# Kernel optimization log

Measured on AMD Instinct MI355X. Metric: run time of the kernel, lower is better.

Reference implementation:

```python
import jax, jax.numpy as jnp
import numpy as np

D = 128          # embedding_dim
L = 3            # gnn layers
P = 100          # num_predicate_classes
C = 50           # num_object_classes
AR = 3           # arity
A = 16           # num_actions
NVB = 200_000    # boolean variables
NVN = 100_000    # numeric variables
NF = 100_000     # factors (objects)
EB = 400_000     # boolean edges
EN = 200_000     # numeric edges


def setup_inputs() -> dict:
    key = jax.random.key(0)
    ks = jax.random.split(key, 24)
    s = 1.0 / np.sqrt(D)
    inp = {
        # boolean subgraph
        "var_type_bool": jax.random.randint(ks[0], (NVB,), 0, P),
        "var_value_bool": jax.random.randint(ks[1], (NVB,), 0, 2),
        # numeric subgraph
        "var_type_num": jax.random.randint(ks[2], (NVN,), 0, P),
        "var_value_num": jax.random.normal(ks[3], (NVN,), dtype=jnp.float32),
        # factors
        "factor_class": jax.random.randint(ks[4], (NF,), 0, C),
        # edges (sender = variable idx, receiver = factor idx, attr = arity slot)
        "senders_bool": jax.random.randint(ks[5], (EB,), 0, NVB),
        "receivers_bool": jax.random.randint(ks[6], (EB,), 0, NF),
        "edge_type_bool": jax.random.randint(ks[7], (EB,), 0, AR),
        "senders_num": jax.random.randint(ks[8], (EN,), 0, NVN),
        "receivers_num": jax.random.randint(ks[9], (EN,), 0, NF),
        "edge_type_num": jax.random.randint(ks[10], (EN,), 0, AR),
        "action_mask": jax.random.randint(ks[11], (NF, A), 0, 2).astype(jnp.bool_),
        # learned parameters
        "pred_emb": jax.random.normal(ks[12], (P, D), dtype=jnp.float32) * s,
        "bool_emb": jax.random.normal(ks[13], (2, D), dtype=jnp.float32) * s,
        "fac_emb": jax.random.normal(ks[14], (C, D), dtype=jnp.float32) * s,
        "edge_emb": jax.random.normal(ks[15], (AR, D), dtype=jnp.float32) * s,
        "num_w": jax.random.normal(ks[16], (D,), dtype=jnp.float32) * s,
        "num_b": jnp.zeros((D,), dtype=jnp.float32),
        "W_msg_vf": jax.random.normal(ks[17], (L, D, D), dtype=jnp.float32) * s,
        "W_upd_f": jax.random.normal(ks[18], (L, 2 * D, D), dtype=jnp.float32) * s,
        "W_msg_fv": jax.random.normal(ks[19], (L, D, D), dtype=jnp.float32) * s,
        "W_upd_v": jax.random.normal(ks[20], (L, 2 * D, D), dtype=jnp.float32) * s,
        "W_pol": jax.random.normal(ks[21], (D, A), dtype=jnp.float32) * s,
        "b_pol": jnp.zeros((A,), dtype=jnp.float32),
    }
    return inp


def reference(var_type_bool, var_value_bool, var_type_num, var_value_num,
              factor_class, senders_bool, receivers_bool, edge_type_bool,
              senders_num, receivers_num, edge_type_num, action_mask,
              pred_emb, bool_emb, fac_emb, edge_emb, num_w, num_b,
              W_msg_vf, W_upd_f, W_msg_fv, W_upd_v, W_pol, b_pol):
    act = jax.nn.relu
    # ---- embed boolean variables: predicate embedding + boolean-value embedding
    v_bool = pred_emb[var_type_bool] + bool_emb[var_value_bool]        # [NVB, D]
    # ---- embed numeric variables: MLP on scalar value + predicate embedding
    v_num = act(var_value_num[:, None] * num_w + num_b) + pred_emb[var_type_num]  # [NVN, D]
    # ---- embed factors and edge attributes
    factors = fac_emb[factor_class]                                    # [NF, D]
    # ---- merge graphs: concat variables, offset numeric senders by n boolean vars
    n_vb = v_bool.shape[0]
    variables = jnp.concatenate([v_bool, v_num], axis=0)               # [NV, D]
    senders = jnp.concatenate([senders_bool, senders_num + n_vb])      # [E]
    receivers = jnp.concatenate([receivers_bool, receivers_num])       # [E]
    edge_attr = edge_emb[jnp.concatenate([edge_type_bool, edge_type_num])]  # [E, D]
    n_var = variables.shape[0]
    n_fac = factors.shape[0]
    # ---- bipartite GNN message passing (variable <-> factor)
    for l in range(L):
        # variable -> factor
        m_vf = act((variables[senders] + edge_attr) @ W_msg_vf[l])      # [E, D]
        agg_f = jax.ops.segment_sum(m_vf, receivers, num_segments=n_fac)
        factors = act(jnp.concatenate([factors, agg_f], axis=-1) @ W_upd_f[l])
        # factor -> variable
        m_fv = act((factors[receivers] + edge_attr) @ W_msg_fv[l])     # [E, D]
        agg_v = jax.ops.segment_sum(m_fv, senders, num_segments=n_var)
        variables = act(jnp.concatenate([variables, agg_v], axis=-1) @ W_upd_v[l])
    # ---- policy head: per-factor action logits, masked
    logits = factors @ W_pol + b_pol                                   # [NF, A]
    NEG = jnp.asarray(-1e9, dtype=logits.dtype)
    return jnp.where(action_mask, logits, NEG)
```

## Files before the change

kernel.cpp:

```cpp
#include <hip/hip_runtime.h>
#include <stdint.h>

#define D 128
#define NACT 16
#define LAYERS 3
#define SCH 8192

typedef __attribute__((ext_vector_type(4))) float f32x4;
typedef __attribute__((ext_vector_type(8))) short short8;

__device__ __forceinline__ unsigned short f2bf(float f) {
  union { float f; unsigned int u; } v; v.f = f;
  return (unsigned short)((v.u + 0x7fffu + ((v.u >> 16) & 1u)) >> 16);
}
__device__ __forceinline__ float bf2f(unsigned short s) {
  union { unsigned int u; float f; } v; v.u = ((unsigned int)s) << 16; return v.f;
}
__device__ __forceinline__ f32x4 mfma16(short8 a, short8 b, f32x4 c) {
  return __builtin_amdgcn_mfma_f32_16x16x32_bf16(a, b, c, 0, 0, 0);
}
__device__ __forceinline__ int SWZ(int row, int byteoff) {
  return (row * 256 + byteoff) ^ ((row & 7) << 4);
}

__device__ __forceinline__ void wave_barrier_lds() {
  asm volatile("s_waitcnt lgkmcnt(0)" ::: "memory");
  __builtin_amdgcn_s_barrier();
  __builtin_amdgcn_sched_barrier(0);
}

__device__ __forceinline__ void accum_edge(unsigned w, unsigned t,
                                           float e00, float e01, float e10, float e11,
                                           float e20, float e21, float& a0, float& a1) {
  float ee0 = (t == 0) ? e00 : ((t == 1) ? e10 : e20);
  float ee1 = (t == 0) ? e01 : ((t == 1) ? e11 : e21);
  float v0 = bf2f((unsigned short)(w & 0xFFFF)) + ee0;
  float v1 = bf2f((unsigned short)(w >> 16)) + ee1;
  a0 += v0 > 0.f ? v0 : 0.f;
  a1 += v1 > 0.f ? v1 : 0.f;
}

__global__ void k_setup(const float* __restrict__ Wvf, const float* __restrict__ Wfv,
                        const float* __restrict__ Wuf, const float* __restrict__ Wuv,
                        const float* __restrict__ Wpol, const float* __restrict__ femb,
                        const float* __restrict__ eemb,
                        const unsigned int* __restrict__ mask, int nMaskWords, int nFemb,
                        unsigned short* __restrict__ WvfT, unsigned short* __restrict__ WfvT,
                        unsigned short* __restrict__ WufT, unsigned short* __restrict__ WuvT,
                        unsigned short* __restrict__ WpT, unsigned short* __restrict__ fembB,
                        float* __restrict__ eWt, int* __restrict__ flag) {
  int tid = blockIdx.x * blockDim.x + threadIdx.x;
  int nthr = gridDim.x * blockDim.x;
  auto packT = [&](const float* src, unsigned short* dst, int Lc, int K, int N) {
    int total = Lc * K * N;
    for (int i = tid; i < total; i += nthr) {
      int l = i / (K * N);
      int rem = i - l * (K * N);
      int n = rem / K;
      int k = rem - n * K;
      dst[i] = f2bf(src[(l * K + k) * N + n]);
    }
  };
  packT(Wvf, WvfT, LAYERS, D, D);
  packT(Wfv, WfvT, LAYERS, D, D);
  packT(Wuf, WufT, LAYERS, 2 * D, D);
  packT(Wuv, WuvT, LAYERS, 2 * D, D);
  packT(Wpol, WpT, 1, D, NACT);
  for (int i = tid; i < nFemb; i += nthr) fembB[i] = f2bf(femb[i]);
  for (int o = tid; o < LAYERS * 2 * 3 * D; o += nthr) {
    int c = o & 127;
    int r = o >> 7;
    int t = r % 3; r /= 3;
    int dir = r & 1;
    int l = r >> 1;
    const float* W = (dir == 0 ? Wvf : Wfv) + (size_t)l * D * D;
    float s = 0.f;
    for (int k = 0; k < D; ++k) s += eemb[t * D + k] * W[k * D + c];
    eWt[o] = s;
  }
  int f = 0;
  for (int i = tid; i < nMaskWords; i += nthr) {
    unsigned w = mask[i];
    if (w > 1u) f |= 1;
    if (w > 0x01010101u) f |= 2;
  }
  if (f) atomicOr(flag, f);
}

__global__ void k_hist2(const int* __restrict__ rb, const int* __restrict__ rn,
                        const int* __restrict__ sb, const int* __restrict__ sn,
                        int EB, int EN, int NVB,
                        int* __restrict__ offR, int* __restrict__ offS) {
  int E = EB + EN;
  for (int e = blockIdx.x * blockDim.x + threadIdx.x; e < E; e += gridDim.x * blockDim.x) {
    int dR = (e < EB) ? rb[e] : rn[e - EB];
    atomicAdd(&offR[dR], 1);
    int dS = (e < EB) ? sb[e] : sn[e - EB] + NVB;
    atomicAdd(&offS[dS], 1);
  }
}

__global__ void k_scan_sums2(const int* __restrict__ offR, int nR, int* __restrict__ bsumR,
                             const int* __restrict__ offS, int nS, int* __restrict__ bsumS,
                             int nbR) {
  __shared__ int ts[256];
  const int* data; int n; int* bsum; int blk;
  if ((int)blockIdx.x < nbR) { data = offR; n = nR; bsum = bsumR; blk = blockIdx.x; }
  else { data = offS; n = nS; bsum = bsumS; blk = blockIdx.x - nbR; }
  int base = blk * SCH;
  int s = 0;
  for (int j = threadIdx.x; j < SCH; j += 256) {
    int i = base + j;
    if (i < n) s += data[i];
  }
  ts[threadIdx.x] = s;
  __syncthreads();
  if (threadIdx.x == 0) {
    int tot = 0;
    for (int i = 0; i < 256; ++i) tot += ts[i];
    bsum[blk] = tot;
  }
}

__global__ void k_scan_top2(int* __restrict__ bsumR, int nbR, int* __restrict__ offRend,
                            int* __restrict__ bsumS, int nbS, int* __restrict__ offSend,
                            int E) {
  if (threadIdx.x == 0) {
    int* bsum = (blockIdx.x == 0) ? bsumR : bsumS;
    int nb = (blockIdx.x == 0) ? nbR : nbS;
    int run = 0;
    for (int i = 0; i < nb; ++i) { int t = bsum[i]; bsum[i] = run; run += t; }
    if (blockIdx.x == 0) *offRend = E; else *offSend = E;
  }
}

__global__ void k_scan_apply2(int* __restrict__ offR, int nR, const int* __restrict__ bsumR,
                              int* __restrict__ offS, int nS, const int* __restrict__ bsumS,
                              int nbR) {
  __shared__ int ts[256];
  int* data; int n; const int* bsum; int blk;
  if ((int)blockIdx.x < nbR) { data = offR; n = nR; bsum = bsumR; blk = blockIdx.x; }
  else { data = offS; n = nS; bsum = bsumS; blk = blockIdx.x - nbR; }
  int base = blk * SCH + threadIdx.x * 32;
  int v[32];
  int s = 0;
#pragma unroll
  for (int j = 0; j < 32; ++j) {
    int i = base + j;
    v[j] = (i < n) ? data[i] : 0;
    s += v[j];
  }
  ts[threadIdx.x] = s;
  __syncthreads();
  if (threadIdx.x == 0) {
    int run = 0;
    for (int i = 0; i < 256; ++i) { int t = ts[i]; ts[i] = run; run += t; }
  }
  __syncthreads();
  int run = bsum[blk] + ts[threadIdx.x];
#pragma unroll
  for (int j = 0; j < 32; ++j) {
    run += v[j];
    int i = base + j;
    if (i < n) data[i] = run;
  }
}

__global__ void k_scatter2(const int* __restrict__ rb, const int* __restrict__ rn,
                           const int* __restrict__ sb, const int* __restrict__ sn,
                           const int* __restrict__ tb, const int* __restrict__ tn,
                           int EB, int EN, int NVB,
                           int* __restrict__ offR, unsigned* __restrict__ pkR,
                           int* __restrict__ offS, unsigned* __restrict__ pkS) {
  int E = EB + EN;
  for (int j = blockIdx.x * blockDim.x + threadIdx.x; j < 2 * E; j += gridDim.x * blockDim.x) {
    int d, s, t; int* off; unsigned* pk;
    if (j < E) {
      off = offR; pk = pkR;
      if (j < EB) { d = rb[j]; s = sb[j]; t = tb[j]; }
      else { int k = j - EB; d = rn[k]; s = sn[k] + NVB; t = tn[k]; }
    } else {
      int k2 = j - E;
      off = offS; pk = pkS;
      if (k2 < EB) { d = sb[k2]; s = rb[k2]; t = tb[k2]; }
      else { int k = k2 - EB; d = sn[k] + NVB; s = rn[k]; t = tn[k]; }
    }
    int pos = atomicAdd(&off[d], -1) - 1;
    pk[pos] = (unsigned)s | ((unsigned)t << 20);
  }
}

__global__ void __launch_bounds__(256)
k_emb_xw(const int* __restrict__ vtb, const int* __restrict__ vvb,
         const int* __restrict__ vtn, const float* __restrict__ vvn,
         const float* __restrict__ pred, const float* __restrict__ bemb,
         const float* __restrict__ numw, const float* __restrict__ numb,
         const unsigned short* __restrict__ WxT,
         unsigned short* __restrict__ vars, unsigned short* __restrict__ xw,
         int nvb, int nv) {
  __shared__ unsigned short LDSO[64 * 128];
  int wid = threadIdx.x >> 6, lane = threadIdx.x & 63;
  int r16 = lane & 15, g = lane >> 4;
  int rbase = blockIdx.x * 64 + wid * 16;
  char* ldso = (char*)LDSO + wid * 16 * 256;
  int c2 = lane * 2;

  float be00 = bemb[c2],     be01 = bemb[c2 + 1];
  float be10 = bemb[D + c2], be11 = bemb[D + c2 + 1];
  float nw0 = numw[c2], nw1 = numw[c2 + 1];
  float nb0 = numb[c2], nb1 = numb[c2 + 1];

  short8 bcur[4], bnxt[4];
#pragma unroll
  for (int ks = 0; ks < 4; ++ks)
    bcur[ks] = *(const short8*)(WxT + r16 * D + ks * 32 + g * 8);

#pragma unroll
  for (int h = 0; h < 2; ++h) {
    int tpA[8], isb[8], bvA[8];
    float vlA[8];
#pragma unroll
    for (int r = 0; r < 8; ++r) {
      int row = rbase + h * 8 + r;
      int rg = row < nv ? row : nv - 1;
      isb[r] = rg < nvb;
      if (isb[r]) { tpA[r] = vtb[rg]; bvA[r] = vvb[rg]; vlA[r] = 0.f; }
      else        { tpA[r] = vtn[rg - nvb]; bvA[r] = 0; vlA[r] = vvn[rg - nvb]; }
    }
#pragma unroll
    for (int r = 0; r < 8; ++r) {
      float2 p = *(const float2*)(pred + (size_t)tpA[r] * D + c2);
      float x0, x1;
      if (isb[r]) {
        x0 = p.x + (bvA[r] ? be10 : be00);
        x1 = p.y + (bvA[r] ? be11 : be01);
      } else {
        float a0 = vlA[r] * nw0 + nb0; a0 = a0 > 0.f ? a0 : 0.f;
        float a1 = vlA[r] * nw1 + nb1; a1 = a1 > 0.f ? a1 : 0.f;
        x0 = p.x + a0;
        x1 = p.y + a1;
      }
      *(unsigned*)(ldso + SWZ(h * 8 + r, lane * 4)) =
          (unsigned)f2bf(x0) | ((unsigned)f2bf(x1) << 16);
    }
  }

#pragma unroll
  for (int i = 0; i < 4; ++i) {
    int lr = i * 4 + g;
    int row = rbase + lr;
    if (row < nv)
      *(short8*)((char*)vars + (size_t)row * 256 + r16 * 16) =
          *(const short8*)(ldso + SWZ(lr, r16 * 16));
  }
  short8 a[4];
#pragma unroll
  for (int ks = 0; ks < 4; ++ks)
    a[ks] = *(const short8*)(ldso + SWZ(r16, ks * 64 + g * 16));

  for (int ct = 0; ct < 8; ++ct) {
    if (ct < 7) {
#pragma unroll
      for (int ks = 0; ks < 4; ++ks)
        bnxt[ks] = *(const short8*)(WxT + ((ct + 1) * 16 + r16) * D + ks * 32 + g * 8);
    }
    f32x4 acc = {0.f, 0.f, 0.f, 0.f};
#pragma unroll
    for (int ks = 0; ks < 4; ++ks) acc = mfma16(a[ks], bcur[ks], acc);
#pragma unroll
    for (int j = 0; j < 4; ++j) {
      int lr = g * 4 + j;
      *(unsigned short*)(ldso + SWZ(lr, (ct * 16 + r16) * 2)) = f2bf(acc[j]);
    }
#pragma unroll
    for (int ks = 0; ks < 4; ++ks) bcur[ks] = bnxt[ks];
  }
#pragma unroll
  for (int i = 0; i < 4; ++i) {
    int lr = i * 4 + g;
    int row = rbase + lr;
    if (row < nv)
      *(short8*)((char*)xw + (size_t)row * 256 + r16 * 16) =
          *(const short8*)(ldso + SWZ(lr, r16 * 16));
  }
}

__global__ void __launch_bounds__(256)
k_agg(const unsigned short* __restrict__ xW, const unsigned* __restrict__ pk,
      const int* __restrict__ off, const float* __restrict__ eW,
      unsigned short* __restrict__ agg, int nDest) {
  int lane = threadIdx.x & 63;
  int c2 = lane * 2;
  int gw = (blockIdx.x * blockDim.x + threadIdx.x) >> 6;
  int nW = (gridDim.x * blockDim.x) >> 6;
  float e00 = eW[c2], e01 = eW[c2 + 1];
  float e10 = eW[D + c2], e11 = eW[D + c2 + 1];
  float e20 = eW[2 * D + c2], e21 = eW[2 * D + c2 + 1];

  int d = gw;
  int b = 0, e = 0;
  if (d < nDest) { b = off[d]; e = off[d + 1]; }
  while (d < nDest) {
    int dn = d + nW;
    int bn = 0, en = 0;
    if (dn < nDest) { bn = off[dn]; en = off[dn + 1]; }
    float a0 = 0.f, a1 = 0.f;
    int i = b;
    for (; i + 4 <= e; i += 4) {
      unsigned p0 = pk[i], p1 = pk[i + 1], p2 = pk[i + 2], p3 = pk[i + 3];
      unsigned w0 = *(const unsigned*)(xW + (size_t)(p0 & 0xFFFFF) * D + c2);
      unsigned w1 = *(const unsigned*)(xW + (size_t)(p1 & 0xFFFFF) * D + c2);
      unsigned w2 = *(const unsigned*)(xW + (size_t)(p2 & 0xFFFFF) * D + c2);
      unsigned w3 = *(const unsigned*)(xW + (size_t)(p3 & 0xFFFFF) * D + c2);
      accum_edge(w0, p0 >> 20, e00, e01, e10, e11, e20, e21, a0, a1);
      accum_edge(w1, p1 >> 20, e00, e01, e10, e11, e20, e21, a0, a1);
      accum_edge(w2, p2 >> 20, e00, e01, e10, e11, e20, e21, a0, a1);
      accum_edge(w3, p3 >> 20, e00, e01, e10, e11, e20, e21, a0, a1);
    }
    if (i + 2 <= e) {
      unsigned p0 = pk[i], p1 = pk[i + 1];
      unsigned w0 = *(const unsigned*)(xW + (size_t)(p0 & 0xFFFFF) * D + c2);
      unsigned w1 = *(const unsigned*)(xW + (size_t)(p1 & 0xFFFFF) * D + c2);
      accum_edge(w0, p0 >> 20, e00, e01, e10, e11, e20, e21, a0, a1);
      accum_edge(w1, p1 >> 20, e00, e01, e10, e11, e20, e21, a0, a1);
      i += 2;
    }
    if (i < e) {
      unsigned p0 = pk[i];
      unsigned w0 = *(const unsigned*)(xW + (size_t)(p0 & 0xFFFFF) * D + c2);
      accum_edge(w0, p0 >> 20, e00, e01, e10, e11, e20, e21, a0, a1);
    }
    *(unsigned*)(agg + (size_t)d * D + c2) = (unsigned)f2bf(a0) | ((unsigned)f2bf(a1) << 16);
    d = dn; b = bn; e = en;
  }
}

template <int SRC, int TAIL, int STORE>
__global__ void __launch_bounds__(256)
k_updxw(const int* __restrict__ fcls, const unsigned short* __restrict__ fembB,
        unsigned short* __restrict__ state, const unsigned short* aggb,
        const unsigned short* __restrict__ WuT, const unsigned short* __restrict__ WxT,
        unsigned short* xwOut, const unsigned short* __restrict__ WpT,
        const float* __restrict__ bpol, const void* __restrict__ maskp,
        const int* __restrict__ flag, float* __restrict__ out, int nRows) {
  __shared__ char STG[2][16 * 512];
  __shared__ unsigned short LDSO[16 * 128];
  int wid = threadIdx.x >> 6, lane = threadIdx.x & 63;
  int r16 = lane & 15, g = lane >> 4;
  int ct0 = wid * 2;
  char* ldso = (char*)LDSO;

  short8 b1[2][8];
#pragma unroll
  for (int c2 = 0; c2 < 2; ++c2)
#pragma unroll
    for (int ks = 0; ks < 8; ++ks)
      b1[c2][ks] = *(const short8*)(WuT + ((ct0 + c2) * 16 + r16) * 256 + ks * 32 + g * 8);

  short8 b2[2][4];
  short8 bp[4];
  float bias = 0.f;
  int fl = 0;
  if (TAIL == 0) {
#pragma unroll
    for (int c2 = 0; c2 < 2; ++c2)
#pragma unroll
      for (int ks = 0; ks < 4; ++ks)
        b2[c2][ks] = *(const short8*)(WxT + ((ct0 + c2) * 16 + r16) * D + ks * 32 + g * 8);
  } else {
#pragma unroll
    for (int ks = 0; ks < 4; ++ks)
      bp[ks] = *(const short8*)(WpT + r16 * D + ks * 32 + g * 8);
    bias = bpol[r16];
    fl = *flag;
  }

  int nChunks = (nRows + 15) >> 4;

  int p0 = wid * 1024 + lane * 16;
  int p1 = p0 + 4096;
  int sr0 = p0 >> 9, so0 = p0 & 511;
  int sr1 = p1 >> 9, so1 = p1 & 511;
  int ld0 = sr0 * 512 + (so0 < 256 ? (so0 ^ ((sr0 & 7) << 4))
                                   : 256 + (((so0 - 256) ^ ((sr0 & 7) << 4))));
  int ld1 = sr1 * 512 + (so1 < 256 ? (so1 ^ ((sr1 & 7) << 4))
                                   : 256 + (((so1 - 256) ^ ((sr1 & 7) << 4))));

  auto srcAddr = [&](int cc, int r, int o) -> const unsigned short* {
    int grow = cc * 16 + r;
    int arg = grow < nRows ? grow : nRows - 1;
    if (o < 256) {
      if (SRC == 0) return fembB + (size_t)fcls[arg] * D + (o >> 1);
      return state + (size_t)arg * D + (o >> 1);
    }
    return aggb + (size_t)arg * D + ((o - 256) >> 1);
  };

  int c = blockIdx.x;
  int cur = 0;
  if (c < nChunks) {
    short8 s0 = *(const short8*)srcAddr(c, sr0, so0);
    short8 s1 = *(const short8*)srcAddr(c, sr1, so1);
    *(short8*)(STG[0] + ld0) = s0;
    *(short8*)(STG[0] + ld1) = s1;
    wave_barrier_lds();
  }

  int swz = (r16 & 7) << 4;
  for (; c < nChunks; c += gridDim.x) {
    int cn = c + gridDim.x;
    short8 sn0, sn1;
    bool havenext = (cn < nChunks);
    if (havenext) {
      sn0 = *(const short8*)srcAddr(cn, sr0, so0);
      sn1 = *(const short8*)srcAddr(cn, sr1, so1);
    }

    const char* stg = STG[cur];
    short8 a[8];
#pragma unroll
    for (int ks = 0; ks < 4; ++ks)
      a[ks] = *(const short8*)(stg + r16 * 512 + ((ks * 64 + g * 16) ^ swz));
#pragma unroll
    for (int ks = 0; ks < 4; ++ks)
      a[4 + ks] = *(const short8*)(stg + r16 * 512 + 256 + ((ks * 64 + g * 16) ^ swz));

    int rbase = c * 16;
    f32x4 acc0 = {0.f, 0.f, 0.f, 0.f}, acc1 = {0.f, 0.f, 0.f, 0.f};
#pragma unroll
    for (int ks = 0; ks < 8; ++ks) {
      acc0 = mfma16(a[ks], b1[0][ks], acc0);
      acc1 = mfma16(a[ks], b1[1][ks], acc1);
    }
#pragma unroll
    for (int j = 0; j < 4; ++j) {
      int lr = g * 4 + j;
      float v0 = acc0[j] > 0.f ? acc0[j] : 0.f;
      float v1 = acc1[j] > 0.f ? acc1[j] : 0.f;
      *(unsigned short*)(ldso + SWZ(lr, (ct0 * 16 + r16) * 2)) = f2bf(v0);
      *(unsigned short*)(ldso + SWZ(lr, ((ct0 + 1) * 16 + r16) * 2)) = f2bf(v1);
    }
    wave_barrier_lds();

    if (TAIL == 0) {
      if (STORE) {
#pragma unroll
        for (int i = 0; i < 4; ++i) {
          int lr = i * 4 + g;
          int row = rbase + lr;
          if (row < nRows)
            *(short8*)((char*)state + (size_t)row * 256 + r16 * 16) =
                *(const short8*)(ldso + SWZ(lr, r16 * 16));
        }
      }
      short8 a2[4];
#pragma unroll
      for (int ks = 0; ks < 4; ++ks)
        a2[ks] = *(const short8*)(ldso + SWZ(r16, ks * 64 + g * 16));
      f32x4 x0 = {0.f, 0.f, 0.f, 0.f}, x1 = {0.f, 0.f, 0.f, 0.f};
#pragma unroll
      for (int ks = 0; ks < 4; ++ks) {
        x0 = mfma16(a2[ks], b2[0][ks], x0);
        x1 = mfma16(a2[ks], b2[1][ks], x1);
      }
#pragma unroll
      for (int j = 0; j < 4; ++j) {
        int row = rbase + g * 4 + j;
        if (row < nRows) {
          xwOut[(size_t)row * D + ct0 * 16 + r16] = f2bf(x0[j]);
          xwOut[(size_t)row * D + (ct0 + 1) * 16 + r16] = f2bf(x1[j]);
        }
      }
    } else {
      if (wid == 0) {
        short8 a2[4];
#pragma unroll
        for (int ks = 0; ks < 4; ++ks)
          a2[ks] = *(const short8*)(ldso + SWZ(r16, ks * 64 + g * 16));
        f32x4 acc = {0.f, 0.f, 0.f, 0.f};
#pragma unroll
        for (int ks = 0; ks < 4; ++ks) acc = mfma16(a2[ks], bp[ks], acc);
#pragma unroll
        for (int j = 0; j < 4; ++j) {
          int grow = rbase + g * 4 + j;
          if (grow < nRows) {
            int mi = grow * NACT + r16;
            bool mv;
            if (fl & 2)      mv = ((const float*)maskp)[mi] != 0.0f;
            else if (fl & 1) mv = ((const unsigned char*)maskp)[mi] != 0;
            else             mv = ((const int*)maskp)[mi] != 0;
            out[mi] = mv ? (acc[j] + bias) : -1e9f;
          }
        }
      }
    }

    if (havenext) {
      *(short8*)(STG[cur ^ 1] + ld0) = sn0;
      *(short8*)(STG[cur ^ 1] + ld1) = sn1;
    }
    wave_barrier_lds();
    cur ^= 1;
  }
}

extern "C" void kernel_launch(void* const* d_in, const int* in_sizes, int n_in,
                              void* d_out, int out_size, void* d_ws, size_t ws_size,
                              hipStream_t stream) {
  const int*   vtb  = (const int*)d_in[0];
  const int*   vvb  = (const int*)d_in[1];
  const int*   vtn  = (const int*)d_in[2];
  const float* vvn  = (const float*)d_in[3];
  const int*   fcls = (const int*)d_in[4];
  const int*   sb   = (const int*)d_in[5];
  const int*   rb   = (const int*)d_in[6];
  const int*   tb   = (const int*)d_in[7];
  const int*   sn   = (const int*)d_in[8];
  const int*   rn   = (const int*)d_in[9];
  const int*   tn   = (const int*)d_in[10];
  const void*  mask = d_in[11];
  const float* pred = (const float*)d_in[12];
  const float* bemb = (const float*)d_in[13];
  const float* femb = (const float*)d_in[14];
  const float* eemb = (const float*)d_in[15];
  const float* numw = (const float*)d_in[16];
  const float* numb = (const float*)d_in[17];
  const float* Wvf  = (const float*)d_in[18];
  const float* Wuf  = (const float*)d_in[19];
  const float* Wfv  = (const float*)d_in[20];
  const float* Wuv  = (const float*)d_in[21];
  const float* Wpol = (const float*)d_in[22];
  const float* bpol = (const float*)d_in[23];

  int NVB = in_sizes[0], NVN = in_sizes[2], NF = in_sizes[4];
  int EB = in_sizes[5], EN = in_sizes[8];
  int NV = NVB + NVN, E = EB + EN;
  int nFemb = in_sizes[14];

  char* ws = (char*)d_ws;
  size_t off_b = 0;
  auto alloc = [&](size_t bytes) -> char* {
    char* p = ws + off_b;
    off_b = (off_b + bytes + 255) & ~(size_t)255;
    return p;
  };
  unsigned short* vars  = (unsigned short*)alloc((size_t)NV * D * 2);
  unsigned short* facs  = (unsigned short*)alloc((size_t)NF * D * 2);
  unsigned short* bufV  = (unsigned short*)alloc((size_t)NV * D * 2);
  unsigned short* bufF  = (unsigned short*)alloc((size_t)NF * D * 2);
  unsigned*       pkR   = (unsigned*)alloc((size_t)E * 4);
  unsigned*       pkS   = (unsigned*)alloc((size_t)E * 4);
  int*            offR  = (int*)alloc((size_t)(NF + 2) * 4);
  int*            offS  = (int*)alloc((size_t)(NV + 2) * 4);
  int*            bsumR = (int*)alloc(256 * 4);
  int*            bsumS = (int*)alloc(256 * 4);
  unsigned short* WvfT  = (unsigned short*)alloc((size_t)LAYERS * D * D * 2);
  unsigned short* WfvT  = (unsigned short*)alloc((size_t)LAYERS * D * D * 2);
  unsigned short* WufT  = (unsigned short*)alloc((size_t)LAYERS * D * 2 * D * 2);
  unsigned short* WuvT  = (unsigned short*)alloc((size_t)LAYERS * D * 2 * D * 2);
  unsigned short* WpT   = (unsigned short*)alloc((size_t)NACT * D * 2);
  unsigned short* fembB = (unsigned short*)alloc((size_t)nFemb * 2);
  float*          eWt   = (float*)alloc((size_t)LAYERS * 2 * 3 * D * 4);
  int*            flag  = (int*)alloc(256);

  hipMemsetAsync(flag, 0, 4, stream);
  k_setup<<<512, 256, 0, stream>>>(Wvf, Wfv, Wuf, Wuv, Wpol, femb, eemb,
                                   (const unsigned int*)mask, NF * NACT / 4, nFemb,
                                   WvfT, WfvT, WufT, WuvT, WpT, fembB, eWt, flag);

  int nbR = (NF + SCH - 1) / SCH;
  int nbS = (NV + SCH - 1) / SCH;
  hipMemsetAsync(offR, 0, (size_t)(NF + 1) * 4, stream);
  hipMemsetAsync(offS, 0, (size_t)(NV + 1) * 4, stream);
  k_hist2<<<2048, 256, 0, stream>>>(rb, rn, sb, sn, EB, EN, NVB, offR, offS);
  k_scan_sums2<<<nbR + nbS, 256, 0, stream>>>(offR, NF, bsumR, offS, NV, bsumS, nbR);
  k_scan_top2<<<2, 64, 0, stream>>>(bsumR, nbR, offR + NF, bsumS, nbS, offS + NV, E);
  k_scan_apply2<<<nbR + nbS, 256, 0, stream>>>(offR, NF, bsumR, offS, NV, bsumS, nbR);
  k_scatter2<<<4096, 256, 0, stream>>>(rb, rn, sb, sn, tb, tn, EB, EN, NVB,
                                       offR, pkR, offS, pkS);

  int gV = (NV + 63) / 64;
  k_emb_xw<<<gV, 256, 0, stream>>>(vtb, vvb, vtn, vvn, pred, bemb, numw, numb,
                                   WvfT, vars, bufV, NVB, NV);

  int gUV = 4096;
  int gUF = 2048;

  k_agg<<<8192, 256, 0, stream>>>(bufV, pkR, offR, eWt + (size_t)(0 * 2 + 0) * 3 * D, bufF, NF);
  k_updxw<0, 0, 1><<<gUF, 256, 0, stream>>>(fcls, fembB, facs, bufF,
                                            WufT + (size_t)0 * D * 2 * D, WfvT + (size_t)0 * D * D,
                                            bufF, WpT, bpol, mask, flag, (float*)d_out, NF);
  k_agg<<<8192, 256, 0, stream>>>(bufF, pkS, offS, eWt + (size_t)(0 * 2 + 1) * 3 * D, bufV, NV);
  k_updxw<1, 0, 1><<<gUV, 256, 0, stream>>>(nullptr, nullptr, vars, bufV,
                                            WuvT + (size_t)0 * D * 2 * D, WvfT + (size_t)1 * D * D,
                                            bufV, WpT, bpol, mask, flag, (float*)d_out, NV);
  k_agg<<<8192, 256, 0, stream>>>(bufV, pkR, offR, eWt + (size_t)(1 * 2 + 0) * 3 * D, bufF, NF);
  k_updxw<1, 0, 1><<<gUF, 256, 0, stream>>>(nullptr, nullptr, facs, bufF,
                                            WufT + (size_t)1 * D * 2 * D, WfvT + (size_t)1 * D * D,
                                            bufF, WpT, bpol, mask, flag, (float*)d_out, NF);
  k_agg<<<8192, 256, 0, stream>>>(bufF, pkS, offS, eWt + (size_t)(1 * 2 + 1) * 3 * D, bufV, NV);
  k_updxw<1, 0, 0><<<gUV, 256, 0, stream>>>(nullptr, nullptr, vars, bufV,
                                            WuvT + (size_t)1 * D * 2 * D, WvfT + (size_t)2 * D * D,
                                            bufV, WpT, bpol, mask, flag, (float*)d_out, NV);
  k_agg<<<8192, 256, 0, stream>>>(bufV, pkR, offR, eWt + (size_t)(2 * 2 + 0) * 3 * D, bufF, NF);
  k_updxw<1, 1, 0><<<gUF, 256, 0, stream>>>(nullptr, nullptr, facs, bufF,
                                            WufT + (size_t)2 * D * 2 * D, nullptr,
                                            nullptr, WpT, bpol, mask, flag, (float*)d_out, NF);
}
```

Measured before the change: 767.7 us.

## Recompute initial variable embeddings in first update and prefetch edge indices in aggregation

The embedding kernel no longer writes the initial variable-state buffer. The first variable-update kernel (new SRC=2 variant) recomputes those embeddings on the fly from the predicate, boolean and numeric tables, which removes a full write and read of the variable state. Separately, the aggregation kernel now fetches the first two packed edge entries and the offsets of the next destination one iteration ahead, to hide load latency. The cost is extra gather arithmetic in the update kernel and higher register pressure in the aggregation loop.

```diff
diff --git a/kernel.cpp b/kernel.cpp
--- a/kernel.cpp
+++ b/kernel.cpp
@@ -196,8 +196,7 @@
          const float* __restrict__ pred, const float* __restrict__ bemb,
          const float* __restrict__ numw, const float* __restrict__ numb,
          const unsigned short* __restrict__ WxT,
-         unsigned short* __restrict__ vars, unsigned short* __restrict__ xw,
-         int nvb, int nv) {
+         unsigned short* __restrict__ xw, int nvb, int nv) {
   __shared__ unsigned short LDSO[64 * 128];
   int wid = threadIdx.x >> 6, lane = threadIdx.x & 63;
   int r16 = lane & 15, g = lane >> 4;
@@ -245,14 +244,6 @@
     }
   }
 
-#pragma unroll
-  for (int i = 0; i < 4; ++i) {
-    int lr = i * 4 + g;
-    int row = rbase + lr;
-    if (row < nv)
-      *(short8*)((char*)vars + (size_t)row * 256 + r16 * 16) =
-          *(const short8*)(ldso + SWZ(lr, r16 * 16));
-  }
   short8 a[4];
 #pragma unroll
   for (int ks = 0; ks < 4; ++ks)
@@ -299,13 +290,40 @@
 
   int d = gw;
   int b = 0, e = 0;
-  if (d < nDest) { b = off[d]; e = off[d + 1]; }
+  unsigned pf0 = 0, pf1 = 0;
+  if (d < nDest) {
+    b = off[d]; e = off[d + 1];
+    if (b < e) pf0 = pk[b];
+    if (b + 1 < e) pf1 = pk[b + 1];
+  }
+  int d1 = d + nW;
+  int bn = 0, en = 0;
+  if (d < nDest && d1 < nDest) { bn = off[d1]; en = off[d1 + 1]; }
+
   while (d < nDest) {
-    int dn = d + nW;
-    int bn = 0, en = 0;
-    if (dn < nDest) { bn = off[dn]; en = off[dn + 1]; }
+    unsigned nf0 = 0, nf1 = 0;
+    if (d1 < nDest) {
+      if (bn < en) nf0 = pk[bn];
+      if (bn + 1 < en) nf1 = pk[bn + 1];
+    }
+    int d2 = d1 + nW;
+    int b2 = 0, e2 = 0;
+    if (d2 < nDest) { b2 = off[d2]; e2 = off[d2 + 1]; }
+
     float a0 = 0.f, a1 = 0.f;
     int i = b;
+    if (i < e) {
+      unsigned w0 = *(const unsigned*)(xW + (size_t)(pf0 & 0xFFFFF) * D + c2);
+      if (i + 1 < e) {
+        unsigned w1 = *(const unsigned*)(xW + (size_t)(pf1 & 0xFFFFF) * D + c2);
+        accum_edge(w0, pf0 >> 20, e00, e01, e10, e11, e20, e21, a0, a1);
+        accum_edge(w1, pf1 >> 20, e00, e01, e10, e11, e20, e21, a0, a1);
+        i += 2;
+      } else {
+        accum_edge(w0, pf0 >> 20, e00, e01, e10, e11, e20, e21, a0, a1);
+        i += 1;
+      }
+    }
     for (; i + 4 <= e; i += 4) {
       unsigned p0 = pk[i], p1 = pk[i + 1], p2 = pk[i + 2], p3 = pk[i + 3];
       unsigned w0 = *(const unsigned*)(xW + (size_t)(p0 & 0xFFFFF) * D + c2);
@@ -331,7 +349,10 @@
       accum_edge(w0, p0 >> 20, e00, e01, e10, e11, e20, e21, a0, a1);
     }
     *(unsigned*)(agg + (size_t)d * D + c2) = (unsigned)f2bf(a0) | ((unsigned)f2bf(a1) << 16);
-    d = dn; b = bn; e = en;
+
+    d = d1; b = bn; e = en;
+    d1 = d2; bn = b2; en = e2;
+    pf0 = nf0; pf1 = nf1;
   }
 }
 
@@ -342,7 +363,11 @@
         const unsigned short* __restrict__ WuT, const unsigned short* __restrict__ WxT,
         unsigned short* xwOut, const unsigned short* __restrict__ WpT,
         const float* __restrict__ bpol, const void* __restrict__ maskp,
-        const int* __restrict__ flag, float* __restrict__ out, int nRows) {
+        const int* __restrict__ flag, float* __restrict__ out, int nRows,
+        const int* __restrict__ vtb2, const int* __restrict__ vvb2,
+        const int* __restrict__ vtn2, const float* __restrict__ vvn2,
+        const float* __restrict__ predp, const float* __restrict__ bembp,
+        const float* __restrict__ numwp, const float* __restrict__ numbp, int nvb2) {
   __shared__ char STG[2][16 * 512];
   __shared__ unsigned short LDSO[16 * 128];
   int wid = threadIdx.x >> 6, lane = threadIdx.x & 63;
@@ -386,21 +411,52 @@
   int ld1 = sr1 * 512 + (so1 < 256 ? (so1 ^ ((sr1 & 7) << 4))
                                    : 256 + (((so1 - 256) ^ ((sr1 & 7) << 4))));
 
-  auto srcAddr = [&](int cc, int r, int o) -> const unsigned short* {
+  auto loadVal = [&](int cc, int r, int o) -> short8 {
     int grow = cc * 16 + r;
     int arg = grow < nRows ? grow : nRows - 1;
     if (o < 256) {
-      if (SRC == 0) return fembB + (size_t)fcls[arg] * D + (o >> 1);
-      return state + (size_t)arg * D + (o >> 1);
-    }
-    return aggb + (size_t)arg * D + ((o - 256) >> 1);
+      if (SRC == 0) return *(const short8*)(fembB + (size_t)fcls[arg] * D + (o >> 1));
+      if (SRC == 1) return *(const short8*)(state + (size_t)arg * D + (o >> 1));
+      int c0 = o >> 1;
+      short8 rv;
+      const float* pp;
+      if (arg < nvb2) {
+        int tp = vtb2[arg], bv = vvb2[arg];
+        pp = predp + (size_t)tp * D + c0;
+        const float* bb = bembp + (size_t)bv * D + c0;
+        f32x4 pa = *(const f32x4*)pp, pb = *(const f32x4*)(pp + 4);
+        f32x4 ba = *(const f32x4*)bb, bb4 = *(const f32x4*)(bb + 4);
+#pragma unroll
+        for (int j = 0; j < 4; ++j) {
+          rv[j] = (short)f2bf(pa[j] + ba[j]);
+          rv[4 + j] = (short)f2bf(pb[j] + bb4[j]);
+        }
+      } else {
+        int jn = arg - nvb2;
+        int tp = vtn2[jn];
+        float v = vvn2[jn];
+        pp = predp + (size_t)tp * D + c0;
+        f32x4 pa = *(const f32x4*)pp, pb = *(const f32x4*)(pp + 4);
+        f32x4 wa = *(const f32x4*)(numwp + c0), wb = *(const f32x4*)(numwp + c0 + 4);
+        f32x4 ca = *(const f32x4*)(numbp + c0), cb = *(const f32x4*)(numbp + c0 + 4);
+#pragma unroll
+        for (int j = 0; j < 4; ++j) {
+          float x0 = v * wa[j] + ca[j]; x0 = x0 > 0.f ? x0 : 0.f;
+          float x1 = v * wb[j] + cb[j]; x1 = x1 > 0.f ? x1 : 0.f;
+          rv[j] = (short)f2bf(x0 + pa[j]);
+          rv[4 + j] = (short)f2bf(x1 + pb[j]);
+        }
+      }
+      return rv;
+    }
+    return *(const short8*)(aggb + (size_t)arg * D + ((o - 256) >> 1));
   };
 
   int c = blockIdx.x;
   int cur = 0;
   if (c < nChunks) {
-    short8 s0 = *(const short8*)srcAddr(c, sr0, so0);
-    short8 s1 = *(const short8*)srcAddr(c, sr1, so1);
+    short8 s0 = loadVal(c, sr0, so0);
+    short8 s1 = loadVal(c, sr1, so1);
     *(short8*)(STG[0] + ld0) = s0;
     *(short8*)(STG[0] + ld1) = s1;
     wave_barrier_lds();
@@ -412,8 +468,8 @@
     short8 sn0, sn1;
     bool havenext = (cn < nChunks);
     if (havenext) {
-      sn0 = *(const short8*)srcAddr(cn, sr0, so0);
-      sn1 = *(const short8*)srcAddr(cn, sr1, so1);
+      sn0 = loadVal(cn, sr0, so0);
+      sn1 = loadVal(cn, sr1, so1);
     }
 
     const char* stg = STG[cur];
@@ -581,7 +637,7 @@
 
   int gV = (NV + 63) / 64;
   k_emb_xw<<<gV, 256, 0, stream>>>(vtb, vvb, vtn, vvn, pred, bemb, numw, numb,
-                                   WvfT, vars, bufV, NVB, NV);
+                                   WvfT, bufV, NVB, NV);
 
   int gUV = 4096;
   int gUF = 2048;
@@ -589,21 +645,30 @@
   k_agg<<<8192, 256, 0, stream>>>(bufV, pkR, offR, eWt + (size_t)(0 * 2 + 0) * 3 * D, bufF, NF);
   k_updxw<0, 0, 1><<<gUF, 256, 0, stream>>>(fcls, fembB, facs, bufF,
                                             WufT + (size_t)0 * D * 2 * D, WfvT + (size_t)0 * D * D,
-                                            bufF, WpT, bpol, mask, flag, (float*)d_out, NF);
+                                            bufF, WpT, bpol, mask, flag, (float*)d_out, NF,
+                                            nullptr, nullptr, nullptr, nullptr,
+                                            nullptr, nullptr, nullptr, nullptr, 0);
   k_agg<<<8192, 256, 0, stream>>>(bufF, pkS, offS, eWt + (size_t)(0 * 2 + 1) * 3 * D, bufV, NV);
-  k_updxw<1, 0, 1><<<gUV, 256, 0, stream>>>(nullptr, nullptr, vars, bufV,
+  k_updxw<2, 0, 1><<<gUV, 256, 0, stream>>>(nullptr, nullptr, vars, bufV,
                                             WuvT + (size_t)0 * D * 2 * D, WvfT + (size_t)1 * D * D,
-                                            bufV, WpT, bpol, mask, flag, (float*)d_out, NV);
+                                            bufV, WpT, bpol, mask, flag, (float*)d_out, NV,
+                                            vtb, vvb, vtn, vvn, pred, bemb, numw, numb, NVB);
   k_agg<<<8192, 256, 0, stream>>>(bufV, pkR, offR, eWt + (size_t)(1 * 2 + 0) * 3 * D, bufF, NF);
   k_updxw<1, 0, 1><<<gUF, 256, 0, stream>>>(nullptr, nullptr, facs, bufF,
                                             WufT + (size_t)1 * D * 2 * D, WfvT + (size_t)1 * D * D,
-                                            bufF, WpT, bpol, mask, flag, (float*)d_out, NF);
+                                            bufF, WpT, bpol, mask, flag, (float*)d_out, NF,
+                                            nullptr, nullptr, nullptr, nullptr,
+                                            nullptr, nullptr, nullptr, nullptr, 0);
   k_agg<<<8192, 256, 0, stream>>>(bufF, pkS, offS, eWt + (size_t)(1 * 2 + 1) * 3 * D, bufV, NV);
   k_updxw<1, 0, 0><<<gUV, 256, 0, stream>>>(nullptr, nullptr, vars, bufV,
                                             WuvT + (size_t)1 * D * 2 * D, WvfT + (size_t)2 * D * D,
-                                            bufV, WpT, bpol, mask, flag, (float*)d_out, NV);
+                                            bufV, WpT, bpol, mask, flag, (float*)d_out, NV,
+                                            nullptr, nullptr, nullptr, nullptr,
+                                            nullptr, nullptr, nullptr, nullptr, 0);
   k_agg<<<8192, 256, 0, stream>>>(bufV, pkR, offR, eWt + (size_t)(2 * 2 + 0) * 3 * D, bufF, NF);
   k_updxw<1, 1, 0><<<gUF, 256, 0, stream>>>(nullptr, nullptr, facs, bufF,
                                             WufT + (size_t)2 * D * 2 * D, nullptr,
-                                            nullptr, WpT, bpol, mask, flag, (float*)d_out, NF);
-}
+                                            nullptr, WpT, bpol, mask, flag, (float*)d_out, NF,
+                                            nullptr, nullptr, nullptr, nullptr,
+                                            nullptr, nullptr, nullptr, nullptr, 0);
+}
```

Result: slower. 873.2 us (+13.7%).
